# Performance work log

Measured on AMD Instinct MI355X. Metric: run time of the kernel, lower is better.

The kernel has to match this reference:

```python
import jax, jax.numpy as jnp
import numpy as np

SEQ_LEN = 720
PRED_LEN = 720
PERIOD = 24
EMB = 64
P_IN = SEQ_LEN // PERIOD            # 30
P_OUT = -(-PRED_LEN // PERIOD)      # 30 (ceil)
FREQ = EMB // 2 + 1                 # 33
DOM = (SEQ_LEN // PERIOD + 1) * 2 + 10  # 72
RATIO = PRED_LEN / SEQ_LEN          # 1.0


def _clin(z, Wr, Wi, br, bi):
    # complex nn.Linear over last dim: z @ W.T + b
    W = Wr + 1j * Wi
    b = br + 1j * bi
    return jnp.einsum('...i,oi->...o', z, W) + b


def _forward(x, freq_Wr, freq_Wi, freq_br, freq_bi, WP_W, WP_b, W_pos,
             mix1_Wr, mix1_Wi, mix1_br, mix1_bi,
             fmix_Wr, fmix_Wi, fmix_br, fmix_bi,
             proj_Wr, proj_Wi, proj_br, proj_bi,
             head_W, head_b):
    B, T, N = x.shape
    # ---- low-frequency branch ----
    low = jnp.fft.rfft(x, axis=1)[:, :DOM, :]               # [B, DOM, N] complex
    low = jnp.swapaxes(low, 1, 2)                           # [B, N, DOM]
    low = _clin(low, freq_Wr, freq_Wi, freq_br, freq_bi)    # [B, N, DOM_out]
    low = jnp.swapaxes(low, 1, 2)                           # [B, DOM_out, N]
    out_bins = PRED_LEN // 2 + 1
    low = jnp.pad(low, ((0, 0), (0, out_bins - low.shape[1]), (0, 0)))
    low_xy = jnp.fft.irfft(low, n=PRED_LEN, axis=1) * RATIO  # [B, PRED_LEN, N]

    # ---- period branch (single fixed period 24; SEQ_LEN % 24 == 0) ----
    xk = jnp.swapaxes(x, 1, 2).reshape(B, N, P_IN, PERIOD)  # unfold(size=step=24)
    xk = jnp.einsum('bnpi,oi->bnpo', xk, WP_W) + WP_b       # [B,N,P_IN,EMB]
    pf = jnp.fft.rfft(xk, axis=-1) + W_pos                  # [B,N,P_IN,FREQ] (W_pos real -> real part)
    pf = jnp.swapaxes(pf, -1, -2)                           # [B,N,FREQ,P_IN]
    o = _clin(pf, mix1_Wr, mix1_Wi, mix1_br, mix1_bi) + pf
    o = jnp.swapaxes(_clin(jnp.swapaxes(o, -1, -2), fmix_Wr, fmix_Wi, fmix_br, fmix_bi), -1, -2) + o
    o = _clin(o, proj_Wr, proj_Wi, proj_br, proj_bi)        # [B,N,FREQ,P_OUT]
    o = jnp.swapaxes(o, -1, -2)                             # [B,N,P_OUT,FREQ]
    pp = jnp.fft.irfft(o, n=EMB, axis=-1).reshape(B, N, P_OUT * EMB)
    pred = jnp.einsum('bnf,of->bno', pp, head_W) + head_b   # [B,N,PRED_LEN]
    pred = jnp.swapaxes(pred, 1, 2)                         # [B,PRED_LEN,N]
    return 0.7 * pred + 0.3 * low_xy


def setup_inputs() -> dict:
    B, N = 128, 128
    ks = jax.random.split(jax.random.key(0), 22)
    f32 = jnp.float32
    def w(k, shape, s=0.05):
        return jax.random.normal(k, shape, dtype=f32) * s
    return {
        'x': jax.random.normal(ks[0], (B, SEQ_LEN, N), dtype=f32),
        'freq_Wr': w(ks[1], (DOM, DOM)), 'freq_Wi': w(ks[2], (DOM, DOM)),
        'freq_br': w(ks[3], (DOM,)), 'freq_bi': w(ks[4], (DOM,)),
        'WP_W': w(ks[5], (EMB, PERIOD)), 'WP_b': w(ks[6], (EMB,)),
        'W_pos': jax.random.uniform(ks[7], (B, N, P_IN, FREQ), dtype=f32, minval=-0.02, maxval=0.02),
        'mix1_Wr': w(ks[8], (P_IN, P_IN)), 'mix1_Wi': w(ks[9], (P_IN, P_IN)),
        'mix1_br': w(ks[10], (P_IN,)), 'mix1_bi': w(ks[11], (P_IN,)),
        'fmix_Wr': w(ks[12], (FREQ, FREQ)), 'fmix_Wi': w(ks[13], (FREQ, FREQ)),
        'fmix_br': w(ks[14], (FREQ,)), 'fmix_bi': w(ks[15], (FREQ,)),
        'proj_Wr': w(ks[16], (P_OUT, P_IN)), 'proj_Wi': w(ks[17], (P_OUT, P_IN)),
        'proj_br': w(ks[18], (P_OUT,)), 'proj_bi': w(ks[19], (P_OUT,)),
        'head_W': w(ks[20], (PRED_LEN, P_OUT * EMB)), 'head_b': w(ks[21], (PRED_LEN,)),
    }


def reference(x, freq_Wr, freq_Wi, freq_br, freq_bi, WP_W, WP_b, W_pos,
              mix1_Wr, mix1_Wi, mix1_br, mix1_bi,
              fmix_Wr, fmix_Wi, fmix_br, fmix_bi,
              proj_Wr, proj_Wi, proj_br, proj_bi,
              head_W, head_b):
    return _forward(x, freq_Wr, freq_Wi, freq_br, freq_bi, WP_W, WP_b, W_pos,
                    mix1_Wr, mix1_Wi, mix1_br, mix1_bi,
                    fmix_Wr, fmix_Wi, fmix_br, fmix_bi,
                    proj_Wr, proj_Wi, proj_br, proj_bi,
                    head_W, head_b)
```

## Files before the change

### kernel.cpp

```cpp
#include <hip/hip_runtime.h>
#include <hip/hip_bf16.h>
#include <math.h>

#define SEQ 720
#define NCH 128
#define BATCH 128
#define BN 16384
#define DOM 72
#define PIN 30
#define POUT 30
#define FRQ 33
#define EMB 64
#define PER 24
#define KW 990
#define KP 1728
#define MT 768
#define PI_F 3.14159265358979323846f

typedef float2 cf;
__device__ __forceinline__ cf cmac(cf acc, cf a, cf b){
  acc.x += a.x*b.x - a.y*b.y; acc.y += a.x*b.y + a.y*b.x; return acc;
}
__device__ __forceinline__ short b2s(float f){
  __hip_bfloat16 h = __float2bfloat16(f);
  return *reinterpret_cast<short*>(&h);
}

__global__ __launch_bounds__(256) void p15(const float* __restrict__ WPW, const float* __restrict__ WPb,
                         const float* __restrict__ m1r, const float* __restrict__ m1i,
                         const float* __restrict__ m1br, const float* __restrict__ m1bi,
                         const float* __restrict__ fxr, const float* __restrict__ fxi,
                         const float* __restrict__ fxbr, const float* __restrict__ fxbi,
                         const float* __restrict__ pjr, const float* __restrict__ pji,
                         const float* __restrict__ pjbr, const float* __restrict__ pjbi,
                         const float* __restrict__ fqr, const float* __restrict__ fqi,
                         cf* C, cf* PM, cf* M2, cf* o3b,
                         float* __restrict__ A1r, float* __restrict__ A1i)
{
  __shared__ cf e64[64];
  __shared__ float sW[EMB*PER];
  __shared__ float sWb[EMB];
  __shared__ float sM1r[PIN*PIN], sM1i[PIN*PIN];
  __shared__ float sFxr[FRQ*FRQ], sFxi[FRQ*FRQ];
  __shared__ float sPjr[POUT*PIN], sPji[POUT*PIN];
  __shared__ float sB[6*33];
  __shared__ cf s_d[FRQ];
  __shared__ cf s_rs[PIN];
  __shared__ cf s_o1[FRQ*PIN];
  __shared__ cf s_o2[FRQ*PIN];
  __shared__ cf tbl[720];
  __shared__ cf wrow[DOM];

  int tid = threadIdx.x;
  if (blockIdx.x < DOM){
    int k = blockIdx.x;
    for (int m=tid;m<720;m+=256){ float s,c; sincosf(-2.f*PI_F*(float)m/720.f,&s,&c); tbl[m]=make_float2(c,s); }
    for (int j=tid;j<DOM;j+=256) wrow[j]=make_float2(fqr[k*DOM+j], fqi[k*DOM+j]);
    __syncthreads();
    for (int tau=tid; tau<720; tau+=256){
      cf acc=make_float2(0.f,0.f);
      for (int j=0;j<DOM;++j) acc = cmac(acc, wrow[j], tbl[(j*tau)%720]);
      A1r[k*720+tau]=acc.x;
      A1i[k*720+tau]=acc.y;
    }
    return;
  }
  if (tid < 64){ float s,c; sincosf(2.f*PI_F*tid/64.f, &s, &c); e64[tid] = make_float2(c, s); }
  for (int i=tid; i<EMB*PER; i+=256) sW[i]=WPW[i];
  if (tid < EMB) sWb[tid]=WPb[tid];
  for (int i=tid; i<PIN*PIN; i+=256){ sM1r[i]=m1r[i]; sM1i[i]=m1i[i]; sPjr[i]=pjr[i]; sPji[i]=pji[i]; }
  for (int i=tid; i<FRQ*FRQ; i+=256){ sFxr[i]=fxr[i]; sFxi[i]=fxi[i]; }
  if (tid < PIN)  { sB[tid]      = m1br[tid]; sB[33+tid]  = m1bi[tid]; }
  if (tid < FRQ)  { sB[66+tid]   = fxbr[tid]; sB[99+tid]  = fxbi[tid]; }
  if (tid < POUT) { sB[132+tid]  = pjbr[tid]; sB[165+tid] = pjbi[tid]; }
  __syncthreads();
  for (int idx=tid; idx<FRQ*PER; idx+=256){
    int f = idx/PER, i = idx%PER;
    cf acc = make_float2(0.f,0.f);
    #pragma unroll 8
    for (int o=0;o<EMB;++o){ cf e = e64[(f*o)&63]; float w = sW[o*PER+i]; acc.x += w*e.x; acc.y -= w*e.y; }
    C[idx] = acc;
  }
  for (int f=tid; f<FRQ; f+=256){
    cf acc = make_float2(0.f,0.f);
    #pragma unroll 8
    for (int o=0;o<EMB;++o){ cf e = e64[(f*o)&63]; acc.x += sWb[o]*e.x; acc.y -= sWb[o]*e.y; }
    s_d[f]=acc;
  }
  for (int idx=tid; idx<POUT*PIN; idx+=256){
    int q = idx/PIN, pp = idx%PIN;
    cf acc = make_float2(sPjr[q*PIN+pp], sPji[q*PIN+pp]);
    #pragma unroll 6
    for (int p=0;p<PIN;++p){
      cf a = make_float2(sPjr[q*PIN+p], sPji[q*PIN+p]);
      cf b = make_float2(sM1r[p*PIN+pp], sM1i[p*PIN+pp]);
      acc = cmac(acc, a, b);
    }
    PM[idx]=acc;
  }
  for (int idx=tid; idx<FRQ*FRQ; idx+=256){
    int f = idx/FRQ, ff = idx%FRQ;
    cf v = make_float2(sFxr[idx], sFxi[idx]); if (f==ff) v.x += 1.f;
    M2[idx]=v;
  }
  for (int p=tid; p<PIN; p+=256){
    cf acc = make_float2(1.f,0.f);
    #pragma unroll 6
    for (int pp=0;pp<PIN;++pp){ acc.x += sM1r[p*PIN+pp]; acc.y += sM1i[p*PIN+pp]; }
    s_rs[p]=acc;
  }
  __syncthreads();
  for (int idx=tid; idx<FRQ*PIN; idx+=256){
    int f = idx/PIN, p = idx%PIN;
    cf v = make_float2(0.f,0.f); v = cmac(v, s_d[f], s_rs[p]);
    v.x += sB[p]; v.y += sB[33+p];
    s_o1[idx]=v;
  }
  __syncthreads();
  for (int idx=tid; idx<FRQ*PIN; idx+=256){
    int f = idx/PIN, p = idx%PIN;
    cf acc = make_float2(sB[66+f], sB[99+f]);
    #pragma unroll 4
    for (int ff=0; ff<FRQ; ++ff){
      cf m2 = make_float2(sFxr[f*FRQ+ff], sFxi[f*FRQ+ff]); if (f==ff) m2.x += 1.f;
      acc = cmac(acc, m2, s_o1[ff*PIN+p]);
    }
    s_o2[idx]=acc;
  }
  __syncthreads();
  for (int idx=tid; idx<FRQ*POUT; idx+=256){
    int f = idx/POUT, q = idx%POUT;
    cf acc = make_float2(sB[132+q], sB[165+q]);
    #pragma unroll 6
    for (int p=0;p<PIN;++p){
      cf a = make_float2(sPjr[q*PIN+p], sPji[q*PIN+p]);
      acc = cmac(acc, a, s_o2[f*PIN+p]);
    }
    o3b[f*POUT+q]=acc;
  }
}

__global__ __launch_bounds__(512) void p_big2(const float* __restrict__ hW,
                    const cf* __restrict__ PM, const cf* __restrict__ M2, const cf* __restrict__ o3b,
                    const cf* __restrict__ Cm,
                    const float* __restrict__ fbr, const float* __restrict__ fbi,
                    const float* __restrict__ headb,
                    float* __restrict__ Mper, __hip_bfloat16* __restrict__ BTm,
                    float* __restrict__ bias){
  __shared__ cf e64[64];
  __shared__ float shw[1920];
  __shared__ cf sHc[990];
  __shared__ cf sV1[990];
  __shared__ cf sPM[POUT*PIN];
  __shared__ cf sM2[FRQ*FRQ];
  __shared__ cf sO3[FRQ*POUT];
  __shared__ float red[512];
  cf* sC = (cf*)shw;
  cf* sV = sHc;
  int tid=threadIdx.x; int t=blockIdx.x;
  if (tid<64){ float s,c; sincosf(2.f*PI_F*tid/64.f,&s,&c); e64[tid]=make_float2(c,s); }
  for (int i=tid;i<1920;i+=512) shw[i]=hW[(size_t)t*1920+i];
  for (int i=tid;i<POUT*PIN;i+=512) sPM[i]=PM[i];
  for (int i=tid;i<FRQ*FRQ;i+=512) sM2[i]=M2[i];
  for (int i=tid;i<FRQ*POUT;i+=512) sO3[i]=o3b[i];
  __syncthreads();
  for (int idx=tid; idx<990; idx+=512){
    int q=idx/FRQ, f=idx%FRQ;
    cf acc=make_float2(0.f,0.f);
    const float* hw = &shw[q*64];
    #pragma unroll 8
    for (int o=0;o<EMB;++o){ cf e=e64[(f*o)&63]; float w=hw[o]; acc.x+=w*e.x; acc.y+=w*e.y; }
    float s=((f==0)||(f==32))?(1.f/64.f):(2.f/64.f);
    sHc[idx]=make_float2(acc.x*s, acc.y*s);
  }
  __syncthreads();
  for (int idx=tid; idx<990; idx+=512){
    int f=idx/PIN, p=idx%PIN;
    cf acc=make_float2(0.f,0.f);
    #pragma unroll 6
    for (int q=0;q<POUT;++q) acc=cmac(acc, sHc[q*FRQ+f], sPM[q*PIN+p]);
    sV1[idx]=acc;
  }
  float part=0.f;
  for (int idx=tid; idx<990; idx+=512){
    int q=idx/FRQ, f=idx%FRQ;
    cf h=sHc[idx]; cf o=sO3[f*POUT+q];
    part += h.x*o.x - h.y*o.y;
  }
  part *= 0.7f;
  if (tid<DOM){
    int m=(tid*t)%720; float s,c; sincosf(2.f*PI_F*(float)m/720.f,&s,&c);
    float sc=(tid==0)?(1.f/720.f):(2.f/720.f);
    part += 0.3f*sc*(c*fbr[tid] - s*fbi[tid]);
  }
  for (int i=tid;i<FRQ*PER;i+=512) sC[i]=Cm[i];
  red[tid]=part; __syncthreads();
  for (int s=256;s>0;s>>=1){ if (tid<s) red[tid]+=red[tid+s]; __syncthreads(); }
  if (tid==0) bias[t] = red[0] + 0.7f*headb[t];
  __syncthreads();
  for (int idx=tid; idx<990; idx+=512){
    int ff=idx/PIN, pp=idx%PIN;
    cf acc=make_float2(0.f,0.f);
    #pragma unroll 4
    for (int f=0;f<FRQ;++f) acc=cmac(acc, sV1[f*PIN+pp], sM2[f*FRQ+ff]);
    sV[idx]=acc;
  }
  __syncthreads();
  for (int tau=tid; tau<720; tau+=512){
    int p0 = tau/PER, i0 = tau - p0*PER;
    float mper=0.f;
    #pragma unroll 4
    for (int f=0; f<FRQ; ++f){ cf v=sV[f*PIN+p0]; cf c=sC[f*PER+i0]; mper += v.x*c.x - v.y*c.y; }
    Mper[(size_t)t*720 + tau] = 0.7f*mper;
  }
  for (int j=tid;j<KP-SEQ;j+=512){
    float v = 0.f;
    if (j < KW){ int p=j/FRQ, f=j-p*FRQ; v = 0.7f * sV[f*PIN+p].x; }
    BTm[(size_t)t*KP + SEQ + j] = __float2bfloat16(v);
  }
}

__global__ __launch_bounds__(256) void p5m2(const float* __restrict__ A1r,
                                            const float* __restrict__ A1i,
                                            const float* __restrict__ Mper,
                                            __hip_bfloat16* __restrict__ BTm){
  __shared__ float sG[16*144];
  __shared__ float sA[144*16];
  int t0 = blockIdx.y*16, tau0 = blockIdx.x*16;
  int tid = threadIdx.x;
  for (int i=tid; i<16*72; i+=256){
    int tt=i/72, k=i%72;
    int m = ((t0+tt)*k) % 720;
    float s,c; sincosf(2.f*PI_F*(float)m/720.f,&s,&c);
    float sc = (k==0)?(1.f/720.f):(2.f/720.f);
    sG[tt*144+k]    = c*sc;
    sG[tt*144+72+k] = s*sc;
  }
  for (int i=tid; i<72*16; i+=256){
    int k=i/16, tc=i%16;
    sA[k*16+tc]      = A1r[k*720+tau0+tc];
    sA[(72+k)*16+tc] = A1i[k*720+tau0+tc];
  }
  __syncthreads();
  int tt=tid/16, tc=tid%16;
  float acc=0.f;
  #pragma unroll 8
  for (int k=0;k<72;++k)
    acc += sG[tt*144+k]*sA[k*16+tc] - sG[tt*144+72+k]*sA[(72+k)*16+tc];
  int t = t0+tt, tau = tau0+tc;
  float mp = Mper[(size_t)t*720 + tau];
  BTm[(size_t)t*KP + tau] = __float2bfloat16(0.3f*acc + mp);
}

__global__ __launch_bounds__(256) void r12(const float* __restrict__ x, const float* __restrict__ Wp,
                                           __hip_bfloat16* __restrict__ Abig){
  __shared__ float tile[64][65];
  int tid=threadIdx.x;
  int blk = blockIdx.x;
  if (blk < 3072){
    int b = blk/24; int rem = blk%24;
    int t0 = (rem>>1)*64, n0 = (rem&1)*64;
    int c = tid & 63, r0 = tid >> 6;
    #pragma unroll
    for (int s=0;s<16;++s){
      int r = r0 + s*4;
      int t = t0 + r;
      tile[r][c] = (t<SEQ) ? x[((size_t)b*SEQ + t)*NCH + n0 + c] : 0.f;
    }
    __syncthreads();
    int nn0 = tid >> 4;
    int tq  = tid & 15;
    int tt  = t0 + tq*4;
    #pragma unroll
    for (int s=0;s<4;++s){
      int nn = nn0 + s*16;
      short4 v;
      v.x = b2s(tile[tq*4+0][nn]);
      v.y = b2s(tile[tq*4+1][nn]);
      v.z = b2s(tile[tq*4+2][nn]);
      v.w = b2s(tile[tq*4+3][nn]);
      __hip_bfloat16* dst = Abig + (size_t)(b*NCH + n0+nn)*KP + tt;
      if (tt+3 < SEQ){
        *reinterpret_cast<short4*>(dst) = v;
      } else {
        short sv[4] = {v.x, v.y, v.z, v.w};
        for (int j=0;j<4;++j) if (tt+j < SEQ) *reinterpret_cast<short*>(dst+j) = sv[j];
      }
    }
    return;
  }
  int j = (tid & 63)*4;
  int lane4 = tid >> 6;
  int bn = (blk - 3072)*4 + lane4;
  const float* src = Wp + (size_t)bn*KW;
  __hip_bfloat16* dstb = Abig + (size_t)bn*KP + SEQ;
  for (int jj = j; jj < KP-SEQ; jj += 256){
    float f0,f1,f2,f3;
    if (jj+3 < KW){
      float2 u = *reinterpret_cast<const float2*>(src+jj);
      float2 w = *reinterpret_cast<const float2*>(src+jj+2);
      f0=u.x; f1=u.y; f2=w.x; f3=w.y;
    } else {
      f0=(jj  <KW)?src[jj  ]:0.f; f1=(jj+1<KW)?src[jj+1]:0.f;
      f2=(jj+2<KW)?src[jj+2]:0.f; f3=(jj+3<KW)?src[jj+3]:0.f;
    }
    short4 v = { b2s(f0), b2s(f1), b2s(f2), b2s(f3) };
    *reinterpret_cast<short4*>(dstb + jj) = v;
  }
}

typedef __attribute__((ext_vector_type(8))) short bfrag_t;
typedef __attribute__((ext_vector_type(4))) float accf_t;
typedef __attribute__((address_space(1))) void gvoid;
typedef __attribute__((address_space(3))) void lvoid;

__device__ __forceinline__ void gload16(const void* g, void* l){
  __builtin_amdgcn_global_load_lds((gvoid*)(g), (lvoid*)(l), 16, 0, 0);
}

__global__ __launch_bounds__(256) void gemm_main(const __hip_bfloat16* __restrict__ BTm,
                                                 const __hip_bfloat16* __restrict__ Abig,
                                                 const float* __restrict__ bias,
                                                 float* __restrict__ out)
{
  __shared__ __hip_bfloat16 At[128*32];
  __shared__ __hip_bfloat16 Bt[128*32];
  int tid = threadIdx.x;
  int lane = tid & 63;
  int wv = tid >> 6;
  int wr = wv >> 1, wc = wv & 1;
  int t0 = blockIdx.y*128, bn0 = blockIdx.x*128;

  accf_t acc[4][4];
  #pragma unroll
  for (int i=0;i<4;++i)
    #pragma unroll
    for (int j=0;j<4;++j) acc[i][j] = (accf_t){0.f,0.f,0.f,0.f};

  int lin0 = tid, lin1 = 256+tid;
  int row0 = lin0>>2, ug0 = (lin0&3) ^ ((row0>>1)&3);
  int row1 = lin1>>2, ug1 = (lin1&3) ^ ((row1>>1)&3);
  const __hip_bfloat16* gA0 = BTm  + (size_t)(t0 +row0)*KP + ug0*8;
  const __hip_bfloat16* gA1 = BTm  + (size_t)(t0 +row1)*KP + ug1*8;
  const __hip_bfloat16* gB0 = Abig + (size_t)(bn0+row0)*KP + ug0*8;
  const __hip_bfloat16* gB1 = Abig + (size_t)(bn0+row1)*KP + ug1*8;
  char* lA0 = (char*)At + lin0*16; char* lA1 = (char*)At + lin1*16;
  char* lB0 = (char*)Bt + lin0*16; char* lB1 = (char*)Bt + lin1*16;

  int g = lane>>4;
  int arow = wr*64 + (lane&15);
  int brow = wc*64 + (lane&15);

  for (int ks=0; ks<KP/32; ++ks){
    int k0 = ks*32;
    gload16(gA0 + k0, lA0);
    gload16(gA1 + k0, lA1);
    gload16(gB0 + k0, lB0);
    gload16(gB1 + k0, lB1);
    __syncthreads();
    bfrag_t af[4], bb[4];
    #pragma unroll
    for (int mi=0;mi<4;++mi){
      int r = arow + mi*16;
      int uu = g ^ ((r>>1)&3);
      af[mi] = *(const bfrag_t*)((const char*)At + r*64 + uu*16);
    }
    #pragma unroll
    for (int ni=0;ni<4;++ni){
      int r = brow + ni*16;
      int uu = g ^ ((r>>1)&3);
      bb[ni] = *(const bfrag_t*)((const char*)Bt + r*64 + uu*16);
    }
    #pragma unroll
    for (int mi=0;mi<4;++mi)
      #pragma unroll
      for (int ni=0;ni<4;++ni)
        acc[mi][ni] = __builtin_amdgcn_mfma_f32_16x16x32_bf16(af[mi], bb[ni], acc[mi][ni], 0, 0, 0);
    __syncthreads();
  }

  #pragma unroll
  for (int mi=0;mi<4;++mi){
    int tbase = t0 + wr*64 + mi*16 + (lane>>4)*4;
    #pragma unroll
    for (int ni=0;ni<4;++ni){
      int col = bn0 + wc*64 + ni*16 + (lane&15);
      int b = col>>7, n = col&127;
      size_t obase = (size_t)b*(SEQ*NCH) + n;
      #pragma unroll
      for (int r=0;r<4;++r){
        int t = tbase + r;
        if (t<SEQ) out[obase + (size_t)t*NCH] = acc[mi][ni][r] + bias[t];
      }
    }
  }
}

extern "C" void kernel_launch(void* const* d_in, const int* in_sizes, int n_in,
                              void* d_out, int out_size, void* d_ws, size_t ws_size,
                              hipStream_t stream)
{
  const float* x     = (const float*)d_in[0];
  const float* fqWr  = (const float*)d_in[1];
  const float* fqWi  = (const float*)d_in[2];
  const float* fqbr  = (const float*)d_in[3];
  const float* fqbi  = (const float*)d_in[4];
  const float* WPW   = (const float*)d_in[5];
  const float* WPb   = (const float*)d_in[6];
  const float* Wpos  = (const float*)d_in[7];
  const float* m1r   = (const float*)d_in[8];
  const float* m1i   = (const float*)d_in[9];
  const float* m1br  = (const float*)d_in[10];
  const float* m1bi  = (const float*)d_in[11];
  const float* fxr   = (const float*)d_in[12];
  const float* fxi   = (const float*)d_in[13];
  const float* fxbr  = (const float*)d_in[14];
  const float* fxbi  = (const float*)d_in[15];
  const float* pjr   = (const float*)d_in[16];
  const float* pji   = (const float*)d_in[17];
  const float* pjbr  = (const float*)d_in[18];
  const float* pjbi  = (const float*)d_in[19];
  const float* headW = (const float*)d_in[20];
  const float* headb = (const float*)d_in[21];

  char* ws = (char*)d_ws;
  size_t off = 0;
  auto alloc = [&](size_t bytes)->void*{ void* p = ws + off; off += (bytes + 255) & ~(size_t)255; return p; };
  __hip_bfloat16* Abig = (__hip_bfloat16*)alloc((size_t)BN*KP*2);
  __hip_bfloat16* BTm  = (__hip_bfloat16*)alloc((size_t)MT*KP*2);
  float* A1r = (float*)alloc((size_t)DOM*720*4);
  float* A1i = (float*)alloc((size_t)DOM*720*4);
  float* Mper= (float*)alloc((size_t)SEQ*720*4);
  cf* C   = (cf*)alloc((size_t)FRQ*PER*8);
  cf* PM  = (cf*)alloc((size_t)POUT*PIN*8);
  cf* M2  = (cf*)alloc((size_t)FRQ*FRQ*8);
  cf* o3b = (cf*)alloc((size_t)FRQ*POUT*8);
  float* bias = (float*)alloc((size_t)SEQ*4);

  p15<<<DOM+1,256,0,stream>>>(WPW,WPb, m1r,m1i,m1br,m1bi, fxr,fxi,fxbr,fxbi, pjr,pji,pjbr,pjbi,
                              fqWr,fqWi, C,PM,M2,o3b, A1r,A1i);
  r12<<<7168,256,0,stream>>>(x, Wpos, Abig);
  p_big2<<<SEQ,512,0,stream>>>(headW, PM, M2, o3b, C, fqbr, fqbi, headb, Mper, BTm, bias);
  p5m2<<<dim3(45,45),256,0,stream>>>(A1r, A1i, Mper, BTm);
  gemm_main<<<dim3(128, 6), 256, 0, stream>>>(BTm, Abig, bias, (float*)d_out);
}
```

Measured before the change: 156.4 us.

## Fuse mid-stage kernels into one launch and fold low-frequency matmul into per-row pass

Merges r12, p_big2 and p5m2 into a single fused_mid kernel with 512-thread blocks that branch on block index. The low-frequency contribution is now computed inline for each output row, reading A1r/A1i straight from global memory, so the Mper intermediate buffer is no longer written and read back. This removes two launches and a global round-trip, and lets the input-conversion work overlap the per-row work. In exchange, every block reserves the largest shared-memory layout, which can lower occupancy for the simple copy blocks, and the inline low-frequency loop does uncached global reads.

```diff
diff --git a/kernel.cpp b/kernel.cpp
--- a/kernel.cpp
+++ b/kernel.cpp
@@ -140,140 +140,124 @@
   }
 }
 
-__global__ __launch_bounds__(512) void p_big2(const float* __restrict__ hW,
+__global__ __launch_bounds__(512) void fused_mid(const float* __restrict__ hW,
                     const cf* __restrict__ PM, const cf* __restrict__ M2, const cf* __restrict__ o3b,
                     const cf* __restrict__ Cm,
                     const float* __restrict__ fbr, const float* __restrict__ fbi,
                     const float* __restrict__ headb,
-                    float* __restrict__ Mper, __hip_bfloat16* __restrict__ BTm,
-                    float* __restrict__ bias){
-  __shared__ cf e64[64];
-  __shared__ float shw[1920];
-  __shared__ cf sHc[990];
-  __shared__ cf sV1[990];
-  __shared__ cf sPM[POUT*PIN];
-  __shared__ cf sM2[FRQ*FRQ];
-  __shared__ cf sO3[FRQ*POUT];
-  __shared__ float red[512];
-  cf* sC = (cf*)shw;
-  cf* sV = sHc;
-  int tid=threadIdx.x; int t=blockIdx.x;
-  if (tid<64){ float s,c; sincosf(2.f*PI_F*tid/64.f,&s,&c); e64[tid]=make_float2(c,s); }
-  for (int i=tid;i<1920;i+=512) shw[i]=hW[(size_t)t*1920+i];
-  for (int i=tid;i<POUT*PIN;i+=512) sPM[i]=PM[i];
-  for (int i=tid;i<FRQ*FRQ;i+=512) sM2[i]=M2[i];
-  for (int i=tid;i<FRQ*POUT;i+=512) sO3[i]=o3b[i];
-  __syncthreads();
-  for (int idx=tid; idx<990; idx+=512){
-    int q=idx/FRQ, f=idx%FRQ;
-    cf acc=make_float2(0.f,0.f);
-    const float* hw = &shw[q*64];
-    #pragma unroll 8
-    for (int o=0;o<EMB;++o){ cf e=e64[(f*o)&63]; float w=hw[o]; acc.x+=w*e.x; acc.y+=w*e.y; }
-    float s=((f==0)||(f==32))?(1.f/64.f):(2.f/64.f);
-    sHc[idx]=make_float2(acc.x*s, acc.y*s);
-  }
-  __syncthreads();
-  for (int idx=tid; idx<990; idx+=512){
-    int f=idx/PIN, p=idx%PIN;
-    cf acc=make_float2(0.f,0.f);
-    #pragma unroll 6
-    for (int q=0;q<POUT;++q) acc=cmac(acc, sHc[q*FRQ+f], sPM[q*PIN+p]);
-    sV1[idx]=acc;
-  }
-  float part=0.f;
-  for (int idx=tid; idx<990; idx+=512){
-    int q=idx/FRQ, f=idx%FRQ;
-    cf h=sHc[idx]; cf o=sO3[f*POUT+q];
-    part += h.x*o.x - h.y*o.y;
-  }
-  part *= 0.7f;
-  if (tid<DOM){
-    int m=(tid*t)%720; float s,c; sincosf(2.f*PI_F*(float)m/720.f,&s,&c);
-    float sc=(tid==0)?(1.f/720.f):(2.f/720.f);
-    part += 0.3f*sc*(c*fbr[tid] - s*fbi[tid]);
-  }
-  for (int i=tid;i<FRQ*PER;i+=512) sC[i]=Cm[i];
-  red[tid]=part; __syncthreads();
-  for (int s=256;s>0;s>>=1){ if (tid<s) red[tid]+=red[tid+s]; __syncthreads(); }
-  if (tid==0) bias[t] = red[0] + 0.7f*headb[t];
-  __syncthreads();
-  for (int idx=tid; idx<990; idx+=512){
-    int ff=idx/PIN, pp=idx%PIN;
-    cf acc=make_float2(0.f,0.f);
-    #pragma unroll 4
-    for (int f=0;f<FRQ;++f) acc=cmac(acc, sV1[f*PIN+pp], sM2[f*FRQ+ff]);
-    sV[idx]=acc;
-  }
-  __syncthreads();
-  for (int tau=tid; tau<720; tau+=512){
-    int p0 = tau/PER, i0 = tau - p0*PER;
-    float mper=0.f;
-    #pragma unroll 4
-    for (int f=0; f<FRQ; ++f){ cf v=sV[f*PIN+p0]; cf c=sC[f*PER+i0]; mper += v.x*c.x - v.y*c.y; }
-    Mper[(size_t)t*720 + tau] = 0.7f*mper;
-  }
-  for (int j=tid;j<KP-SEQ;j+=512){
-    float v = 0.f;
-    if (j < KW){ int p=j/FRQ, f=j-p*FRQ; v = 0.7f * sV[f*PIN+p].x; }
-    BTm[(size_t)t*KP + SEQ + j] = __float2bfloat16(v);
-  }
-}
-
-__global__ __launch_bounds__(256) void p5m2(const float* __restrict__ A1r,
-                                            const float* __restrict__ A1i,
-                                            const float* __restrict__ Mper,
-                                            __hip_bfloat16* __restrict__ BTm){
-  __shared__ float sG[16*144];
-  __shared__ float sA[144*16];
-  int t0 = blockIdx.y*16, tau0 = blockIdx.x*16;
+                    const float* __restrict__ A1r, const float* __restrict__ A1i,
+                    const float* __restrict__ x, const float* __restrict__ Wp,
+                    __hip_bfloat16* __restrict__ BTm, float* __restrict__ bias,
+                    __hip_bfloat16* __restrict__ Abig){
+  __shared__ double smem_d[6336];
+  char* smem = (char*)smem_d;
   int tid = threadIdx.x;
-  for (int i=tid; i<16*72; i+=256){
-    int tt=i/72, k=i%72;
-    int m = ((t0+tt)*k) % 720;
-    float s,c; sincosf(2.f*PI_F*(float)m/720.f,&s,&c);
-    float sc = (k==0)?(1.f/720.f):(2.f/720.f);
-    sG[tt*144+k]    = c*sc;
-    sG[tt*144+72+k] = s*sc;
-  }
-  for (int i=tid; i<72*16; i+=256){
-    int k=i/16, tc=i%16;
-    sA[k*16+tc]      = A1r[k*720+tau0+tc];
-    sA[(72+k)*16+tc] = A1i[k*720+tau0+tc];
-  }
-  __syncthreads();
-  int tt=tid/16, tc=tid%16;
-  float acc=0.f;
-  #pragma unroll 8
-  for (int k=0;k<72;++k)
-    acc += sG[tt*144+k]*sA[k*16+tc] - sG[tt*144+72+k]*sA[(72+k)*16+tc];
-  int t = t0+tt, tau = tau0+tc;
-  float mp = Mper[(size_t)t*720 + tau];
-  BTm[(size_t)t*KP + tau] = __float2bfloat16(0.3f*acc + mp);
-}
-
-__global__ __launch_bounds__(256) void r12(const float* __restrict__ x, const float* __restrict__ Wp,
-                                           __hip_bfloat16* __restrict__ Abig){
-  __shared__ float tile[64][65];
-  int tid=threadIdx.x;
   int blk = blockIdx.x;
-  if (blk < 3072){
-    int b = blk/24; int rem = blk%24;
+
+  if (blk < SEQ){
+    cf*    e64 = (cf*)(smem + 0);
+    float* shw = (float*)(smem + 512);
+    cf*    sHc = (cf*)(smem + 8192);
+    cf*    sV1 = (cf*)(smem + 16112);
+    cf*    sPM = (cf*)(smem + 24032);
+    cf*    sM2 = (cf*)(smem + 31232);
+    cf*    sO3 = (cf*)(smem + 39944);
+    float* red = (float*)(smem + 47864);
+    float* sG  = (float*)(smem + 49912);
+    cf* sC = (cf*)shw;
+    cf* sV = sHc;
+    int t = blk;
+    if (tid<64){ float s,c; sincosf(2.f*PI_F*tid/64.f,&s,&c); e64[tid]=make_float2(c,s); }
+    if (tid<DOM){
+      int m=(tid*t)%720; float s,c; sincosf(2.f*PI_F*(float)m/720.f,&s,&c);
+      float sc=(tid==0)?(1.f/720.f):(2.f/720.f);
+      sG[tid]=c*sc; sG[72+tid]=s*sc;
+    }
+    for (int i=tid;i<1920;i+=512) shw[i]=hW[(size_t)t*1920+i];
+    for (int i=tid;i<POUT*PIN;i+=512) sPM[i]=PM[i];
+    for (int i=tid;i<FRQ*FRQ;i+=512) sM2[i]=M2[i];
+    for (int i=tid;i<FRQ*POUT;i+=512) sO3[i]=o3b[i];
+    __syncthreads();
+    for (int idx=tid; idx<990; idx+=512){
+      int q=idx/FRQ, f=idx%FRQ;
+      cf acc=make_float2(0.f,0.f);
+      const float* hw = &shw[q*64];
+      #pragma unroll 8
+      for (int o=0;o<EMB;++o){ cf e=e64[(f*o)&63]; float w=hw[o]; acc.x+=w*e.x; acc.y+=w*e.y; }
+      float s=((f==0)||(f==32))?(1.f/64.f):(2.f/64.f);
+      sHc[idx]=make_float2(acc.x*s, acc.y*s);
+    }
+    __syncthreads();
+    for (int idx=tid; idx<990; idx+=512){
+      int f=idx/PIN, p=idx%PIN;
+      cf acc=make_float2(0.f,0.f);
+      #pragma unroll 6
+      for (int q=0;q<POUT;++q) acc=cmac(acc, sHc[q*FRQ+f], sPM[q*PIN+p]);
+      sV1[idx]=acc;
+    }
+    float part=0.f;
+    for (int idx=tid; idx<990; idx+=512){
+      int q=idx/FRQ, f=idx%FRQ;
+      cf h=sHc[idx]; cf o=sO3[f*POUT+q];
+      part += h.x*o.x - h.y*o.y;
+    }
+    part *= 0.7f;
+    if (tid<DOM){
+      int m=(tid*t)%720; float s,c; sincosf(2.f*PI_F*(float)m/720.f,&s,&c);
+      float sc=(tid==0)?(1.f/720.f):(2.f/720.f);
+      part += 0.3f*sc*(c*fbr[tid] - s*fbi[tid]);
+    }
+    for (int i=tid;i<FRQ*PER;i+=512) sC[i]=Cm[i];
+    red[tid]=part; __syncthreads();
+    for (int s=256;s>0;s>>=1){ if (tid<s) red[tid]+=red[tid+s]; __syncthreads(); }
+    if (tid==0) bias[t] = red[0] + 0.7f*headb[t];
+    __syncthreads();
+    for (int idx=tid; idx<990; idx+=512){
+      int ff=idx/PIN, pp=idx%PIN;
+      cf acc=make_float2(0.f,0.f);
+      #pragma unroll 4
+      for (int f=0;f<FRQ;++f) acc=cmac(acc, sV1[f*PIN+pp], sM2[f*FRQ+ff]);
+      sV[idx]=acc;
+    }
+    __syncthreads();
+    for (int tau=tid; tau<720; tau+=512){
+      int p0 = tau/PER, i0 = tau - p0*PER;
+      float mper=0.f;
+      #pragma unroll 4
+      for (int f=0; f<FRQ; ++f){ cf v=sV[f*PIN+p0]; cf c=sC[f*PER+i0]; mper += v.x*c.x - v.y*c.y; }
+      float mlow=0.f;
+      #pragma unroll 8
+      for (int k=0;k<DOM;++k)
+        mlow += sG[k]*A1r[k*720+tau] - sG[72+k]*A1i[k*720+tau];
+      BTm[(size_t)t*KP + tau] = __float2bfloat16(0.3f*mlow + 0.7f*mper);
+    }
+    for (int j=tid;j<KP-SEQ;j+=512){
+      float v = 0.f;
+      if (j < KW){ int p=j/FRQ, f=j-p*FRQ; v = 0.7f * sV[f*PIN+p].x; }
+      BTm[(size_t)t*KP + SEQ + j] = __float2bfloat16(v);
+    }
+    return;
+  }
+
+  if (blk < SEQ + 3072){
+    float (*tile)[65] = (float(*)[65])smem;
+    int bb = blk - SEQ;
+    int b = bb/24; int rem = bb%24;
     int t0 = (rem>>1)*64, n0 = (rem&1)*64;
     int c = tid & 63, r0 = tid >> 6;
     #pragma unroll
-    for (int s=0;s<16;++s){
-      int r = r0 + s*4;
+    for (int s=0;s<8;++s){
+      int r = r0 + s*8;
       int t = t0 + r;
       tile[r][c] = (t<SEQ) ? x[((size_t)b*SEQ + t)*NCH + n0 + c] : 0.f;
     }
     __syncthreads();
+    int tq  = tid & 15;
     int nn0 = tid >> 4;
-    int tq  = tid & 15;
     int tt  = t0 + tq*4;
     #pragma unroll
-    for (int s=0;s<4;++s){
-      int nn = nn0 + s*16;
+    for (int s=0;s<2;++s){
+      int nn = nn0 + s*32;
       short4 v;
       v.x = b2s(tile[tq*4+0][nn]);
       v.y = b2s(tile[tq*4+1][nn]);
@@ -289,23 +273,27 @@
     }
     return;
   }
-  int j = (tid & 63)*4;
-  int lane4 = tid >> 6;
-  int bn = (blk - 3072)*4 + lane4;
-  const float* src = Wp + (size_t)bn*KW;
-  __hip_bfloat16* dstb = Abig + (size_t)bn*KP + SEQ;
-  for (int jj = j; jj < KP-SEQ; jj += 256){
-    float f0,f1,f2,f3;
-    if (jj+3 < KW){
-      float2 u = *reinterpret_cast<const float2*>(src+jj);
-      float2 w = *reinterpret_cast<const float2*>(src+jj+2);
-      f0=u.x; f1=u.y; f2=w.x; f3=w.y;
-    } else {
-      f0=(jj  <KW)?src[jj  ]:0.f; f1=(jj+1<KW)?src[jj+1]:0.f;
-      f2=(jj+2<KW)?src[jj+2]:0.f; f3=(jj+3<KW)?src[jj+3]:0.f;
-    }
-    short4 v = { b2s(f0), b2s(f1), b2s(f2), b2s(f3) };
-    *reinterpret_cast<short4*>(dstb + jj) = v;
+
+  {
+    int bb = blk - SEQ - 3072;
+    int lane8 = tid >> 6;
+    int bn = bb*8 + lane8;
+    int j = (tid & 63)*4;
+    const float* src = Wp + (size_t)bn*KW;
+    __hip_bfloat16* dstb = Abig + (size_t)bn*KP + SEQ;
+    for (int jj = j; jj < KP-SEQ; jj += 256){
+      float f0,f1,f2,f3;
+      if (jj+3 < KW){
+        float2 u = *reinterpret_cast<const float2*>(src+jj);
+        float2 w = *reinterpret_cast<const float2*>(src+jj+2);
+        f0=u.x; f1=u.y; f2=w.x; f3=w.y;
+      } else {
+        f0=(jj  <KW)?src[jj  ]:0.f; f1=(jj+1<KW)?src[jj+1]:0.f;
+        f2=(jj+2<KW)?src[jj+2]:0.f; f3=(jj+3<KW)?src[jj+3]:0.f;
+      }
+      short4 v = { b2s(f0), b2s(f1), b2s(f2), b2s(f3) };
+      *reinterpret_cast<short4*>(dstb + jj) = v;
+    }
   }
 }
 
@@ -430,7 +418,6 @@
   __hip_bfloat16* BTm  = (__hip_bfloat16*)alloc((size_t)MT*KP*2);
   float* A1r = (float*)alloc((size_t)DOM*720*4);
   float* A1i = (float*)alloc((size_t)DOM*720*4);
-  float* Mper= (float*)alloc((size_t)SEQ*720*4);
   cf* C   = (cf*)alloc((size_t)FRQ*PER*8);
   cf* PM  = (cf*)alloc((size_t)POUT*PIN*8);
   cf* M2  = (cf*)alloc((size_t)FRQ*FRQ*8);
@@ -439,8 +426,7 @@
 
   p15<<<DOM+1,256,0,stream>>>(WPW,WPb, m1r,m1i,m1br,m1bi, fxr,fxi,fxbr,fxbi, pjr,pji,pjbr,pjbi,
                               fqWr,fqWi, C,PM,M2,o3b, A1r,A1i);
-  r12<<<7168,256,0,stream>>>(x, Wpos, Abig);
-  p_big2<<<SEQ,512,0,stream>>>(headW, PM, M2, o3b, C, fqbr, fqbi, headb, Mper, BTm, bias);
-  p5m2<<<dim3(45,45),256,0,stream>>>(A1r, A1i, Mper, BTm);
+  fused_mid<<<SEQ+3072+2048,512,0,stream>>>(headW, PM, M2, o3b, C, fqbr, fqbi, headb,
+                                            A1r, A1i, x, Wpos, BTm, bias, Abig);
   gemm_main<<<dim3(128, 6), 256, 0, stream>>>(BTm, Abig, bias, (float*)d_out);
 }
```

New measurement: 147.8 us. 5.5% less time.
